# Kernel optimization log

Measured on AMD Instinct MI355X. Metric: run time of the kernel, lower is better.

## Reference

```python
import jax, jax.numpy as jnp
import numpy as np

P = 4   # patch_size
H = 8   # num_heads


def setup_inputs() -> dict:
    key = jax.random.key(0)
    k0, k1, k2 = jax.random.split(key, 3)
    B, C, R = 8, 8, 64
    E = C * P ** 3  # 512
    s = 1.0 / np.sqrt(E)
    x = jax.random.normal(k0, (B, C, R, R, R), jnp.float32)
    in_proj_w = jax.random.normal(k1, (3 * E, E), jnp.float32) * s
    in_proj_b = jnp.zeros((3 * E,), jnp.float32)
    out_proj_w = jax.random.normal(k2, (E, E), jnp.float32) * s
    out_proj_b = jnp.zeros((E,), jnp.float32)
    return {"x": x, "in_proj_w": in_proj_w, "in_proj_b": in_proj_b,
            "out_proj_w": out_proj_w, "out_proj_b": out_proj_b}


def reference(x, in_proj_w, in_proj_b, out_proj_w, out_proj_b):
    B, C, Rx, Ry, Rz = x.shape
    p = P
    nx, ny, nz = Rx // p, Ry // p, Rz // p
    N = nx * ny * nz
    E = C * p ** 3
    dh = E // H

    # cyclic shift: move last patch to front == roll by +p on each spatial axis
    x = jnp.roll(x, (p, p, p), axis=(2, 3, 4))

    # window partition: (B,C,nx,p,ny,p,nz,p) -> (B, N, C*p^3), matching
    # unfold + flatten + permute + flatten of the torch code
    xw = (x.reshape(B, C, nx, p, ny, p, nz, p)
           .transpose(0, 2, 4, 6, 1, 3, 5, 7)
           .reshape(B, N, E))

    # nn.MultiheadAttention with batch_first=False: seq dim = B, batch dim = N
    qkv = jnp.einsum('bne,fe->bnf', xw, in_proj_w) + in_proj_b  # (B, N, 3E)
    q, k, v = jnp.split(qkv, 3, axis=-1)
    q = q.reshape(B, N, H, dh)
    k = k.reshape(B, N, H, dh)
    v = v.reshape(B, N, H, dh)
    scale = 1.0 / np.sqrt(dh)
    # attention over the B (sequence) axis, independently per window n and head h
    att = jax.nn.softmax(jnp.einsum('inhd,jnhd->nhij', q * scale, k), axis=-1)
    o = jnp.einsum('nhij,jnhd->inhd', att, v).reshape(B, N, E)
    o = jnp.einsum('bne,fe->bnf', o, out_proj_w) + out_proj_b  # (B, N, E)

    # torch reassembly via the cat-of-permute loops interleaves windows:
    # out[b, c, px*nx + ix, py*ny + iy, pz*nz + iz] = y[b, ix, iy, iz, c, px, py, pz]
    y = (o.reshape(B, nx, ny, nz, C, p, p, p)
          .transpose(0, 4, 5, 1, 6, 2, 7, 3)
          .reshape(B, C, Rx, Ry, Rz))

    # reverse cyclic shift: roll by -p on each spatial axis
    y = jnp.roll(y, (-p, -p, -p), axis=(2, 3, 4))
    return y
```

## Files before the change

kernel.cpp:

```cpp
#include <hip/hip_runtime.h>

typedef unsigned short u16;
typedef unsigned int u32;
typedef __bf16 bf16x8 __attribute__((ext_vector_type(8)));
typedef float f32x16 __attribute__((ext_vector_type(16)));

__device__ __forceinline__ u16 f2bf(float f) {
  u32 u = __builtin_bit_cast(u32, f);
  u = (u + 0x7FFFu + ((u >> 16) & 1u)) >> 16;
  return (u16)u;
}
__device__ __forceinline__ float bf2f(u16 h) {
  u32 u = ((u32)h) << 16;
  return __builtin_bit_cast(float, u);
}

#define GLD16(gp, lp) __builtin_amdgcn_global_load_lds( \
    (const __attribute__((address_space(1))) u32*)(const void*)(gp), \
    (__attribute__((address_space(3))) u32*)(void*)(lp), 16, 0, 0)
#define SBAR() __builtin_amdgcn_s_barrier()
#define SCHED0() __builtin_amdgcn_sched_barrier(0)

__global__ __launch_bounds__(256) void cast_both(const float* __restrict__ w_in,
                                                 u16* __restrict__ wq,
                                                 const float* __restrict__ w_out,
                                                 u16* __restrict__ wo) {
  int i = blockIdx.x * 256 + threadIdx.x;
  const float* src = w_in; u16* dst = wq; int idx = i;
  if (i >= 196608) { src = w_out; dst = wo; idx = i - 196608; }
  float4 v = *(const float4*)(src + (size_t)idx * 4);
  ushort4 u;
  u.x = f2bf(v.x); u.y = f2bf(v.y); u.z = f2bf(v.z); u.w = f2bf(v.w);
  *(ushort4*)(dst + (size_t)idx * 4) = u;
}

__global__ __launch_bounds__(256) void permute_in(const float* __restrict__ x,
                                                  u16* __restrict__ xw) {
  __shared__ float lds[128 * 64];
  int t = threadIdx.x;
  int bx = blockIdx.x;
  int b = blockIdx.y;
  int jx = bx >> 4, jy = bx & 15;
#pragma unroll
  for (int it = 0; it < 8; ++it) {
    int idx = t + it * 256;
    int row = idx >> 4, z4 = idx & 15;
    int c = row >> 4, qx = (row >> 2) & 3, qy = row & 3;
    int X = (jx * 4 + qx + 60) & 63;
    int Y = (jy * 4 + qy + 60) & 63;
    float4 v = *(const float4*)(x + ((((size_t)(b * 8 + c) * 64 + X) * 64 + Y) * 64 + z4 * 4));
    *(float4*)(lds + row * 64 + ((z4 ^ (row & 7)) << 2)) = v;
  }
  __syncthreads();
#pragma unroll
  for (int it = 0; it < 8; ++it) {
    int idx = t + it * 256;
    int jz = idx >> 7, r = idx & 127;
    int z4r = (jz + 15) & 15;
    float4 v = *(const float4*)(lds + r * 64 + ((z4r ^ (r & 7)) << 2));
    int nw = jx * 256 + jy * 16 + jz;
    ushort4 u;
    u.x = f2bf(v.x); u.y = f2bf(v.y); u.z = f2bf(v.z); u.w = f2bf(v.w);
    *(ushort4*)(xw + (size_t)(nw * 8 + b) * 512 + r * 4) = u;
  }
}

__global__ __launch_bounds__(256, 2) void gemm_qkv_attn(const u16* __restrict__ A,
                                                        const u16* __restrict__ W,
                                                        const float* __restrict__ bias,
                                                        u16* __restrict__ O) {
  __shared__ u16 smem[40960];
  u16* As = smem;
  u16* Bs = smem + 16384;
  float* ctf = (float*)smem;

  int cpx = gridDim.x >> 3;
  int wg = (blockIdx.x & 7) * cpx + (blockIdx.x >> 3);
  int mbc = wg >> 3, h = wg & 7;
  int m0 = mbc * 128;

  int tid = threadIdx.x;
  int wv = tid >> 6, l = tid & 63;
  int wr = wv >> 1, wc = wv & 1;
  int l31 = l & 31, g = l >> 5;

  int kch = ((l & 3) ^ ((l >> 3) & 3)) * 8;
  const u16* pa[2]; int dA[2];
#pragma unroll
  for (int i = 0; i < 2; ++i) {
    int slot = wv * 128 + i * 64 + l;
    int row = slot >> 2;
    pa[i] = A + (size_t)(m0 + row) * 512 + kch;
    dA[i] = (wv * 128 + i * 64) * 8;
  }
  const u16* pb[3]; int dB[3];
#pragma unroll
  for (int i = 0; i < 3; ++i) {
    int slot = wv * 192 + i * 64 + l;
    int row = slot >> 2;
    int grow = (row >> 6) * 512 + h * 64 + (row & 63);
    pb[i] = W + (size_t)grow * 512 + kch;
    dB[i] = (wv * 192 + i * 64) * 8;
  }

  int abase[2], bbase[3];
#pragma unroll
  for (int m = 0; m < 2; ++m) abase[m] = (wr * 64 + m * 32 + l31) * 32;
#pragma unroll
  for (int n = 0; n < 3; ++n) bbase[n] = (wc * 96 + n * 32 + l31) * 32;
  int rsw = (l31 >> 1) & 3;

  f32x16 acc[2][3] = {};

#pragma unroll
  for (int ts = 0; ts < 3; ++ts) {
    int kadd = ts * 32;
    GLD16(pa[0] + kadd, As + ts * 4096 + dA[0]);
    GLD16(pa[1] + kadd, As + ts * 4096 + dA[1]);
    GLD16(pb[0] + kadd, Bs + ts * 6144 + dB[0]);
    GLD16(pb[1] + kadd, Bs + ts * 6144 + dB[1]);
    GLD16(pb[2] + kadd, Bs + ts * 6144 + dB[2]);
  }
  asm volatile("s_waitcnt vmcnt(10)" ::: "memory");
  SCHED0(); SBAR(); SCHED0();

  for (int t = 0; t < 16; ++t) {
    const u16* AsT = As + (t & 3) * 4096;
    const u16* BsT = Bs + (t & 3) * 6144;
    u16* Ad = As + ((t + 3) & 3) * 4096;
    u16* Bd = Bs + ((t + 3) & 3) * 6144;
    int nx = (t + 3) * 32;
    bool st = t + 3 < 16;
#pragma unroll
    for (int s = 0; s < 2; ++s) {
      int cofs = ((((s << 1) | g) ^ rsw)) << 3;
      bf16x8 af[2], bf[3];
      af[0] = *(const bf16x8*)(AsT + abase[0] + cofs);
      af[1] = *(const bf16x8*)(AsT + abase[1] + cofs);
      bf[0] = *(const bf16x8*)(BsT + bbase[0] + cofs);
      bf[1] = *(const bf16x8*)(BsT + bbase[1] + cofs);
      bf[2] = *(const bf16x8*)(BsT + bbase[2] + cofs);
      if (s == 0 && st) { GLD16(pa[0] + nx, Ad + dA[0]); GLD16(pa[1] + nx, Ad + dA[1]); }
      if (s == 1 && st) {
        GLD16(pb[0] + nx, Bd + dB[0]); GLD16(pb[1] + nx, Bd + dB[1]);
        GLD16(pb[2] + nx, Bd + dB[2]);
      }
      SCHED0();
      __builtin_amdgcn_s_setprio(1);
#pragma unroll
      for (int m = 0; m < 2; ++m)
#pragma unroll
        for (int n = 0; n < 3; ++n)
          acc[m][n] = __builtin_amdgcn_mfma_f32_32x32x16_bf16(bf[n], af[m], acc[m][n], 0, 0, 0);
      __builtin_amdgcn_s_setprio(0);
      SCHED0();
    }
    if (t <= 12) {
      asm volatile("s_waitcnt vmcnt(10)" ::: "memory");
    } else if (t == 13) {
      asm volatile("s_waitcnt vmcnt(5)" ::: "memory");
    } else if (t == 14) {
      asm volatile("s_waitcnt vmcnt(0)" ::: "memory");
    }
    SCHED0();
    if (t < 15) { SBAR(); SCHED0(); }
  }

  __syncthreads();

#pragma unroll
  for (int c = 0; c < 4; ++c) {
    if ((c >> 1) == wr) {
      const int m = c & 1;
      int skey = ((l31 >> 3) & 3) << 2;
#pragma unroll
      for (int n = 0; n < 3; ++n)
#pragma unroll
        for (int q = 0; q < 4; ++q) {
          int col0 = wc * 96 + n * 32 + q * 8 + g * 4;
          int gcol = ((col0 >> 6) << 9) + (h << 6) + (col0 & 63);
          float4 bv = *(const float4*)(bias + gcol);
          float4 stv;
          stv.x = acc[m][n][q * 4 + 0] + bv.x;
          stv.y = acc[m][n][q * 4 + 1] + bv.y;
          stv.z = acc[m][n][q * 4 + 2] + bv.z;
          stv.w = acc[m][n][q * 4 + 3] + bv.w;
          *(float4*)(ctf + l31 * 204 + (col0 ^ skey)) = stv;
        }
    }
    __syncthreads();
    {
      int qi = l >> 3, j = l & 7;
      int K4 = wv << 2;
      const float* qr = ctf + (wv * 8 + qi) * 204;
      const float* kr = ctf + (wv * 8 + j) * 204;
      float sc = 0.f;
#pragma unroll
      for (int d = 0; d < 16; ++d) {
        float4 qv = *(const float4*)(qr + ((d * 4) ^ K4));
        float4 kv = *(const float4*)(kr + ((64 + d * 4) ^ K4));
        sc += qv.x * kv.x + qv.y * kv.y + qv.z * kv.z + qv.w * kv.w;
      }
      sc *= 0.125f;
      float mx = sc;
      mx = fmaxf(mx, __shfl_xor(mx, 1));
      mx = fmaxf(mx, __shfl_xor(mx, 2));
      mx = fmaxf(mx, __shfl_xor(mx, 4));
      float p = __expf(sc - mx);
      float sum = p;
      sum += __shfl_xor(sum, 1);
      sum += __shfl_xor(sum, 2);
      sum += __shfl_xor(sum, 4);
      p /= sum;
      float pr[8];
      int lb = l & 56;
#pragma unroll
      for (int jj = 0; jj < 8; ++jj) pr[jj] = __shfl(p, lb + jj);
      float ov[8] = {};
#pragma unroll
      for (int jj = 0; jj < 8; ++jj) {
        const float* vr = ctf + (wv * 8 + jj) * 204;
        int b0 = 128 + j * 8;
        float4 va = *(const float4*)(vr + (b0 ^ K4));
        float4 vb = *(const float4*)(vr + ((b0 + 4) ^ K4));
        float pj = pr[jj];
        ov[0] += pj * va.x; ov[1] += pj * va.y; ov[2] += pj * va.z; ov[3] += pj * va.w;
        ov[4] += pj * vb.x; ov[5] += pj * vb.y; ov[6] += pj * vb.z; ov[7] += pj * vb.w;
      }
      ushort4 r0, r1;
      r0.x = f2bf(ov[0]); r0.y = f2bf(ov[1]); r0.z = f2bf(ov[2]); r0.w = f2bf(ov[3]);
      r1.x = f2bf(ov[4]); r1.y = f2bf(ov[5]); r1.z = f2bf(ov[6]); r1.w = f2bf(ov[7]);
      u16* dst = O + (size_t)(m0 + c * 32 + wv * 8 + qi) * 512 + h * 64 + j * 8;
      *(ushort4*)dst = r0;
      *(ushort4*)(dst + 4) = r1;
    }
    __syncthreads();
  }
}

__global__ __launch_bounds__(512, 4) void gemm_out(const u16* __restrict__ A,
                                                   const u16* __restrict__ Wt,
                                                   const float* __restrict__ bias,
                                                   u16* __restrict__ C) {
  __shared__ u16 smem[24576];
  u16* As = smem;
  u16* Bs = smem + 16384;

  int cpx = gridDim.x >> 3;
  int wg = (blockIdx.x & 7) * cpx + (blockIdx.x >> 3);
  int mb = wg >> 2, nb = wg & 3;
  int m0 = mb * 256, n0 = nb * 128;

  int tid = threadIdx.x;
  int wv = tid >> 6, l = tid & 63;
  int wr = wv >> 1, wc = wv & 1;
  int l31 = l & 31, g = l >> 5;

  int kch = ((l & 3) ^ ((l >> 3) & 3)) * 8;
  const u16* pa[2]; int dA[2];
#pragma unroll
  for (int i = 0; i < 2; ++i) {
    int slot = wv * 128 + i * 64 + l;
    int row = slot >> 2;
    pa[i] = A + (size_t)(m0 + row) * 512 + kch;
    dA[i] = (wv * 128 + i * 64) * 8;
  }
  int slotB = wv * 64 + l;
  int rowB = slotB >> 2;
  const u16* pb = Wt + (size_t)(n0 + rowB) * 512 + kch;
  int dB = (wv * 64) * 8;

  int abase[2], bbase[2];
#pragma unroll
  for (int m = 0; m < 2; ++m) abase[m] = (wr * 64 + m * 32 + l31) * 32;
#pragma unroll
  for (int n = 0; n < 2; ++n) bbase[n] = (wc * 64 + n * 32 + l31) * 32;
  int rsw = (l31 >> 1) & 3;

  f32x16 acc[2][2] = {};

  GLD16(pa[0], As + dA[0]); GLD16(pa[1], As + dA[1]);
  GLD16(pb, Bs + dB);
  asm volatile("s_waitcnt vmcnt(0)" ::: "memory");
  SCHED0(); SBAR(); SCHED0();

  for (int t = 0; t < 16; ++t) {
    const u16* AsT = As + (t & 1) * 8192;
    const u16* BsT = Bs + (t & 1) * 4096;
    u16* Ad = As + ((t + 1) & 1) * 8192;
    u16* Bd = Bs + ((t + 1) & 1) * 4096;
    int nx = (t + 1) * 32;
    bool st = t < 15;
#pragma unroll
    for (int s = 0; s < 2; ++s) {
      int cofs = ((((s << 1) | g) ^ rsw)) << 3;
      bf16x8 af[2], bf[2];
      af[0] = *(const bf16x8*)(AsT + abase[0] + cofs);
      af[1] = *(const bf16x8*)(AsT + abase[1] + cofs);
      bf[0] = *(const bf16x8*)(BsT + bbase[0] + cofs);
      bf[1] = *(const bf16x8*)(BsT + bbase[1] + cofs);
      if (s == 0 && st) { GLD16(pa[0] + nx, Ad + dA[0]); GLD16(pa[1] + nx, Ad + dA[1]); }
      if (s == 1 && st) { GLD16(pb + nx, Bd + dB); }
      SCHED0();
      __builtin_amdgcn_s_setprio(1);
#pragma unroll
      for (int m = 0; m < 2; ++m)
#pragma unroll
        for (int n = 0; n < 2; ++n)
          acc[m][n] = __builtin_amdgcn_mfma_f32_32x32x16_bf16(bf[n], af[m], acc[m][n], 0, 0, 0);
      __builtin_amdgcn_s_setprio(0);
      SCHED0();
    }
    asm volatile("s_waitcnt vmcnt(0)" ::: "memory");
    SCHED0(); SBAR(); SCHED0();
  }

#pragma unroll
  for (int m = 0; m < 2; ++m) {
    size_t row = (size_t)(m0 + wr * 64 + m * 32 + l31);
#pragma unroll
    for (int n = 0; n < 2; ++n)
#pragma unroll
      for (int q = 0; q < 4; ++q) {
        int col0 = n0 + wc * 64 + n * 32 + q * 8 + g * 4;
        float4 bv = *(const float4*)(bias + col0);
        ushort4 uu;
        uu.x = f2bf(acc[m][n][q * 4 + 0] + bv.x);
        uu.y = f2bf(acc[m][n][q * 4 + 1] + bv.y);
        uu.z = f2bf(acc[m][n][q * 4 + 2] + bv.z);
        uu.w = f2bf(acc[m][n][q * 4 + 3] + bv.w);
        *(ushort4*)(C + row * 512 + col0) = uu;
      }
  }
}

__global__ __launch_bounds__(256) void permute_out(const u16* __restrict__ o2,
                                                   float* __restrict__ out) {
  __shared__ float lds[16 * 516];
  int t = threadIdx.x;
  int bx = blockIdx.x;
  int b = blockIdx.y;
  int ix = bx >> 4, iy = bx & 15;
  int n0 = ix * 256 + iy * 16;
#pragma unroll
  for (int it = 0; it < 8; ++it) {
    int idx = t + it * 256;
    int iz = idx >> 7, fq = idx & 127;
    ushort4 u = *(const ushort4*)(o2 + ((size_t)((n0 + iz) * 8 + b) * 512 + fq * 4));
    float4 v;
    v.x = bf2f(u.x); v.y = bf2f(u.y); v.z = bf2f(u.z); v.w = bf2f(u.w);
    *(float4*)(lds + iz * 516 + fq * 4) = v;
  }
  __syncthreads();
#pragma unroll
  for (int it = 0; it < 8; ++it) {
    int idx = t + it * 256;
    int fidx = idx >> 4, w4 = idx & 15;
    int c = fidx >> 4, px = (fidx >> 2) & 3, py = fidx & 3;
    int W0 = (w4 * 4 + 4) & 63;
    int pz = W0 >> 4, iz0 = W0 & 15;
    int fa = fidx * 4 + pz;
    float4 v;
    v.x = lds[(iz0 + 0) * 516 + fa];
    v.y = lds[(iz0 + 1) * 516 + fa];
    v.z = lds[(iz0 + 2) * 516 + fa];
    v.w = lds[(iz0 + 3) * 516 + fa];
    int uu = (px * 16 + ix + 60) & 63;
    int vv = (py * 16 + iy + 60) & 63;
    *(float4*)(out + ((((size_t)(b * 8 + c) * 64 + uu) * 64 + vv) * 64 + w4 * 4)) = v;
  }
}

extern "C" void kernel_launch(void* const* d_in, const int* in_sizes, int n_in,
                              void* d_out, int out_size, void* d_ws, size_t ws_size,
                              hipStream_t stream) {
  const float* x     = (const float*)d_in[0];
  const float* w_in  = (const float*)d_in[1];
  const float* b_in  = (const float*)d_in[2];
  const float* w_out = (const float*)d_in[3];
  const float* b_out = (const float*)d_in[4];
  float* out = (float*)d_out;

  char* ws = (char*)d_ws;
  u16* wq  = (u16*)(ws);
  u16* wo  = (u16*)(ws + 1572864);
  u16* xw2 = (u16*)(ws + 2097152);
  u16* o   = (u16*)(ws + 35651584);
  u16* o2  = (u16*)(ws + 69206016);

  cast_both<<<1024, 256, 0, stream>>>(w_in, wq, w_out, wo);
  permute_in<<<dim3(256, 8), 256, 0, stream>>>(x, xw2);
  gemm_qkv_attn<<<2048, 256, 0, stream>>>(xw2, wq, b_in, o);
  gemm_out<<<512, 512, 0, stream>>>(o, wo, b_out, o2);
  permute_out<<<dim3(256, 8), 256, 0, stream>>>(o2, out);
}
```

Measured before the change: 158.0 us.

## Enlarge QKV-attention GEMM tile to 256 rows with 512-thread blocks and 16x16 MFMA

The fused QKV GEMM and attention kernel now processes 256 rows per block with 8 waves, where it previously used 128 rows with 4 waves. The MFMA shape changes from 32x32x16 to 16x16x32, and the B tile is reused across more rows, so weight traffic per output drops. Extra barriers and lgkmcnt waits are added inside each k-step, which may cost synchronization. Only half the waves run the attention stage per chunk, and the grid is halved.

```diff
diff --git a/kernel.cpp b/kernel.cpp
--- a/kernel.cpp
+++ b/kernel.cpp
@@ -3,6 +3,7 @@
 typedef unsigned short u16;
 typedef unsigned int u32;
 typedef __bf16 bf16x8 __attribute__((ext_vector_type(8)));
+typedef float f32x4 __attribute__((ext_vector_type(4)));
 typedef float f32x16 __attribute__((ext_vector_type(16)));
 
 __device__ __forceinline__ u16 f2bf(float f) {
@@ -20,6 +21,7 @@
     (__attribute__((address_space(3))) u32*)(void*)(lp), 16, 0, 0)
 #define SBAR() __builtin_amdgcn_s_barrier()
 #define SCHED0() __builtin_amdgcn_sched_barrier(0)
+#define LGKM0() asm volatile("s_waitcnt lgkmcnt(0)" ::: "memory")
 
 __global__ __launch_bounds__(256) void cast_both(const float* __restrict__ w_in,
                                                  u16* __restrict__ wq,
@@ -65,131 +67,142 @@
   }
 }
 
-__global__ __launch_bounds__(256, 2) void gemm_qkv_attn(const u16* __restrict__ A,
+__global__ __launch_bounds__(512, 2) void gemm_qkv_attn(const u16* __restrict__ A,
                                                         const u16* __restrict__ W,
                                                         const float* __restrict__ bias,
                                                         u16* __restrict__ O) {
-  __shared__ u16 smem[40960];
+  __shared__ u16 smem[57344];
   u16* As = smem;
-  u16* Bs = smem + 16384;
+  u16* Bs = smem + 32768;
   float* ctf = (float*)smem;
 
   int cpx = gridDim.x >> 3;
   int wg = (blockIdx.x & 7) * cpx + (blockIdx.x >> 3);
   int mbc = wg >> 3, h = wg & 7;
-  int m0 = mbc * 128;
+  int m0 = mbc * 256;
 
   int tid = threadIdx.x;
   int wv = tid >> 6, l = tid & 63;
-  int wr = wv >> 1, wc = wv & 1;
-  int l31 = l & 31, g = l >> 5;
-
-  int kch = ((l & 3) ^ ((l >> 3) & 3)) * 8;
-  const u16* pa[2]; int dA[2];
-#pragma unroll
-  for (int i = 0; i < 2; ++i) {
-    int slot = wv * 128 + i * 64 + l;
-    int row = slot >> 2;
-    pa[i] = A + (size_t)(m0 + row) * 512 + kch;
-    dA[i] = (wv * 128 + i * 64) * 8;
-  }
-  const u16* pb[3]; int dB[3];
-#pragma unroll
-  for (int i = 0; i < 3; ++i) {
-    int slot = wv * 192 + i * 64 + l;
-    int row = slot >> 2;
-    int grow = (row >> 6) * 512 + h * 64 + (row & 63);
-    pb[i] = W + (size_t)grow * 512 + kch;
-    dB[i] = (wv * 192 + i * 64) * 8;
-  }
-
-  int abase[2], bbase[3];
-#pragma unroll
-  for (int m = 0; m < 2; ++m) abase[m] = (wr * 64 + m * 32 + l31) * 32;
-#pragma unroll
-  for (int n = 0; n < 3; ++n) bbase[n] = (wc * 96 + n * 32 + l31) * 32;
-  int rsw = (l31 >> 1) & 3;
-
-  f32x16 acc[2][3] = {};
+  int wr = wv >> 2, wc = wv & 3;
+  int lr = l & 15, lg = l >> 4;
+  bool half0 = (tid < 256);
+
+  int sA0 = tid, sA1 = 512 + tid;
+  int ch0 = ((sA0 & 3) ^ ((sA0 >> 3) & 3)) * 8;
+  int ch1 = ((sA1 & 3) ^ ((sA1 >> 3) & 3)) * 8;
+  const u16* pa0 = A + (size_t)(m0 + (sA0 >> 2)) * 512 + ch0;
+  const u16* pa1 = A + (size_t)(m0 + (sA1 >> 2)) * 512 + ch1;
+  int rB0 = sA0 >> 2;
+  int rB1 = sA1 >> 2;
+  const u16* pb0 = W + (size_t)((rB0 >> 6) * 512 + h * 64 + (rB0 & 63)) * 512 + ch0;
+  const u16* pb1 = W + (size_t)((rB1 >> 6) * 512 + h * 64 + (rB1 & 63)) * 512 + ch1;
+  int dA0 = (wv * 64) * 8;
+  int dA1 = (512 + wv * 64) * 8;
+
+  int cofs = (lg ^ ((lr >> 1) & 3)) * 8;
+  int arow = (wr * 128 + lr) * 32;
+  int brow = (wc * 48 + lr) * 32;
+
+  f32x4 acc[8][3] = {};
 
 #pragma unroll
   for (int ts = 0; ts < 3; ++ts) {
-    int kadd = ts * 32;
-    GLD16(pa[0] + kadd, As + ts * 4096 + dA[0]);
-    GLD16(pa[1] + kadd, As + ts * 4096 + dA[1]);
-    GLD16(pb[0] + kadd, Bs + ts * 6144 + dB[0]);
-    GLD16(pb[1] + kadd, Bs + ts * 6144 + dB[1]);
-    GLD16(pb[2] + kadd, Bs + ts * 6144 + dB[2]);
-  }
-  asm volatile("s_waitcnt vmcnt(10)" ::: "memory");
+    int ka = ts * 32, sl = ts;
+    GLD16(pa0 + ka, As + sl * 8192 + dA0);
+    GLD16(pa1 + ka, As + sl * 8192 + dA1);
+    GLD16(pb0 + ka, Bs + sl * 6144 + dA0);
+    if (half0) GLD16(pb1 + ka, Bs + sl * 6144 + dA1);
+  }
+  if (half0) { asm volatile("s_waitcnt vmcnt(8)" ::: "memory"); }
+  else       { asm volatile("s_waitcnt vmcnt(6)" ::: "memory"); }
   SCHED0(); SBAR(); SCHED0();
 
   for (int t = 0; t < 16; ++t) {
-    const u16* AsT = As + (t & 3) * 4096;
+    const u16* AsT = As + (t & 3) * 8192;
     const u16* BsT = Bs + (t & 3) * 6144;
-    u16* Ad = As + ((t + 3) & 3) * 4096;
-    u16* Bd = Bs + ((t + 3) & 3) * 6144;
-    int nx = (t + 3) * 32;
-    bool st = t + 3 < 16;
-#pragma unroll
-    for (int s = 0; s < 2; ++s) {
-      int cofs = ((((s << 1) | g) ^ rsw)) << 3;
-      bf16x8 af[2], bf[3];
-      af[0] = *(const bf16x8*)(AsT + abase[0] + cofs);
-      af[1] = *(const bf16x8*)(AsT + abase[1] + cofs);
-      bf[0] = *(const bf16x8*)(BsT + bbase[0] + cofs);
-      bf[1] = *(const bf16x8*)(BsT + bbase[1] + cofs);
-      bf[2] = *(const bf16x8*)(BsT + bbase[2] + cofs);
-      if (s == 0 && st) { GLD16(pa[0] + nx, Ad + dA[0]); GLD16(pa[1] + nx, Ad + dA[1]); }
-      if (s == 1 && st) {
-        GLD16(pb[0] + nx, Bd + dB[0]); GLD16(pb[1] + nx, Bd + dB[1]);
-        GLD16(pb[2] + nx, Bd + dB[2]);
-      }
+    int sl = (t + 3) & 3;
+    u16* Ad = As + sl * 8192;
+    u16* Bd = Bs + sl * 6144;
+    int ka = (t + 3) * 32;
+    bool st = (t + 3) < 16;
+    bf16x8 bf[3];
+#pragma unroll
+    for (int p = 0; p < 4; ++p) {
+      bf16x8 af[2];
+      af[0] = *(const bf16x8*)(AsT + arow + (p * 2 + 0) * 512 + cofs);
+      af[1] = *(const bf16x8*)(AsT + arow + (p * 2 + 1) * 512 + cofs);
+      if (p == 0) {
+        bf[0] = *(const bf16x8*)(BsT + brow + 0 * 512 + cofs);
+        bf[1] = *(const bf16x8*)(BsT + brow + 1 * 512 + cofs);
+        bf[2] = *(const bf16x8*)(BsT + brow + 2 * 512 + cofs);
+      }
+      if (st) {
+        if (p == 0) GLD16(pa0 + ka, Ad + dA0);
+        if (p == 1) GLD16(pa1 + ka, Ad + dA1);
+        if (p == 2) GLD16(pb0 + ka, Bd + dA0);
+        if (p == 3 && half0) GLD16(pb1 + ka, Bd + dA1);
+      }
+      SCHED0();
+      SBAR();
+      LGKM0();
       SCHED0();
       __builtin_amdgcn_s_setprio(1);
 #pragma unroll
-      for (int m = 0; m < 2; ++m)
+      for (int mm = 0; mm < 2; ++mm)
 #pragma unroll
         for (int n = 0; n < 3; ++n)
-          acc[m][n] = __builtin_amdgcn_mfma_f32_32x32x16_bf16(bf[n], af[m], acc[m][n], 0, 0, 0);
+          acc[p * 2 + mm][n] = __builtin_amdgcn_mfma_f32_16x16x32_bf16(
+              bf[n], af[mm], acc[p * 2 + mm][n], 0, 0, 0);
       __builtin_amdgcn_s_setprio(0);
       SCHED0();
+      if (p == 3) {
+        if (t <= 12) {
+          if (half0) { asm volatile("s_waitcnt vmcnt(8)" ::: "memory"); }
+          else       { asm volatile("s_waitcnt vmcnt(6)" ::: "memory"); }
+        } else if (t == 13) {
+          if (half0) { asm volatile("s_waitcnt vmcnt(4)" ::: "memory"); }
+          else       { asm volatile("s_waitcnt vmcnt(3)" ::: "memory"); }
+        } else if (t == 14) {
+          asm volatile("s_waitcnt vmcnt(0)" ::: "memory");
+        }
+        SCHED0();
+      }
+      SBAR();
     }
-    if (t <= 12) {
-      asm volatile("s_waitcnt vmcnt(10)" ::: "memory");
-    } else if (t == 13) {
-      asm volatile("s_waitcnt vmcnt(5)" ::: "memory");
-    } else if (t == 14) {
-      asm volatile("s_waitcnt vmcnt(0)" ::: "memory");
-    }
-    SCHED0();
-    if (t < 15) { SBAR(); SCHED0(); }
   }
 
   __syncthreads();
 
-#pragma unroll
-  for (int c = 0; c < 4; ++c) {
-    if ((c >> 1) == wr) {
-      const int m = c & 1;
-      int skey = ((l31 >> 3) & 3) << 2;
-#pragma unroll
-      for (int n = 0; n < 3; ++n)
-#pragma unroll
-        for (int q = 0; q < 4; ++q) {
-          int col0 = wc * 96 + n * 32 + q * 8 + g * 4;
-          int gcol = ((col0 >> 6) << 9) + (h << 6) + (col0 & 63);
-          float4 bv = *(const float4*)(bias + gcol);
+  float4 bvv[3];
+#pragma unroll
+  for (int n = 0; n < 3; ++n) {
+    int col0 = wc * 48 + n * 16 + lg * 4;
+    int gcol = ((col0 >> 6) << 9) + (h << 6) + (col0 & 63);
+    bvv[n] = *(const float4*)(bias + gcol);
+  }
+
+#pragma unroll
+  for (int c = 0; c < 8; ++c) {
+    if ((c >> 2) == wr) {
+#pragma unroll
+      for (int mm = 0; mm < 2; ++mm) {
+        const int m = (c & 3) * 2 + mm;
+        int row_local = mm * 16 + lr;
+        int skey = ((row_local >> 3) & 3) << 2;
+#pragma unroll
+        for (int n = 0; n < 3; ++n) {
+          int col0 = wc * 48 + n * 16 + lg * 4;
           float4 stv;
-          stv.x = acc[m][n][q * 4 + 0] + bv.x;
-          stv.y = acc[m][n][q * 4 + 1] + bv.y;
-          stv.z = acc[m][n][q * 4 + 2] + bv.z;
-          stv.w = acc[m][n][q * 4 + 3] + bv.w;
-          *(float4*)(ctf + l31 * 204 + (col0 ^ skey)) = stv;
+          stv.x = acc[m][n][0] + bvv[n].x;
+          stv.y = acc[m][n][1] + bvv[n].y;
+          stv.z = acc[m][n][2] + bvv[n].z;
+          stv.w = acc[m][n][3] + bvv[n].w;
+          *(float4*)(ctf + row_local * 204 + (col0 ^ skey)) = stv;
         }
+      }
     }
     __syncthreads();
-    {
+    if (wv < 4) {
       int qi = l >> 3, j = l & 7;
       int K4 = wv << 2;
       const float* qr = ctf + (wv * 8 + qi) * 204;
@@ -390,7 +403,7 @@
 
   cast_both<<<1024, 256, 0, stream>>>(w_in, wq, w_out, wo);
   permute_in<<<dim3(256, 8), 256, 0, stream>>>(x, xw2);
-  gemm_qkv_attn<<<2048, 256, 0, stream>>>(xw2, wq, b_in, o);
+  gemm_qkv_attn<<<1024, 512, 0, stream>>>(xw2, wq, b_in, o);
   gemm_out<<<512, 512, 0, stream>>>(o, wo, b_out, o2);
   permute_out<<<dim3(256, 8), 256, 0, stream>>>(o2, out);
 }
```

Result: slower. 177.5 us (+12.3%).
